# Performance work log

Hardware: AMD Instinct MI355X
Metric: run time of the kernel (lower is better)

The kernel has to match this reference:

```python
import jax, jax.numpy as jnp
import numpy as np

NUM_HEADS = 16


def _rope_tables(seq_len, head_dim, dtype):
    # angles[n, j] = n * 10000^(-2j/head_dim)
    pos = jnp.arange(seq_len, dtype=jnp.float32)
    inv = jnp.power(10000.0, -2.0 * jnp.arange(head_dim // 2, dtype=jnp.float32) / head_dim)
    ang = pos[:, None] * inv[None, :]                     # [N, D/2]
    # repeat_interleave(.., 2): [c0,c0,c1,c1,...]
    cos = jnp.repeat(jnp.cos(ang), 2, axis=-1).astype(dtype)  # [N, D]
    sin = jnp.repeat(jnp.sin(ang), 2, axis=-1).astype(dtype)  # [N, D]
    return cos[None, None], sin[None, None]               # [1,1,N,D]


def _rotate_half_interleaved(x):
    # stack([-x[...,1::2], x[...,::2]], -1).reshape_as(x)
    x2 = jnp.stack([-x[..., 1::2], x[..., ::2]], axis=-1)
    return x2.reshape(x.shape)


def setup_inputs() -> dict:
    key = jax.random.key(0)
    k0, k1, k2, k3 = jax.random.split(key, 4)
    B, N, C = 2, 2048, 1024
    s = 1.0 / np.sqrt(C)
    return {
        "x": jax.random.normal(k0, (B, N, C), dtype=jnp.float32),
        "Wq": jax.random.normal(k1, (C, C), dtype=jnp.float32) * s,
        "Wk": jax.random.normal(k2, (C, C), dtype=jnp.float32) * s,
        "Wv": jax.random.normal(k3, (C, C), dtype=jnp.float32) * s,
    }


def reference(x, Wq, Wk, Wv):
    B, N, C = x.shape
    H = NUM_HEADS
    D = C // H
    scale = D ** -0.5

    def heads(y):  # [B,N,C] -> [B,H,N,D]
        return y.reshape(B, N, H, D).transpose(0, 2, 1, 3)

    # nn.Linear: y = x @ W.T
    q = heads(x @ Wq.T)
    k = heads(x @ Wk.T)
    v = heads(x @ Wv.T)

    cos, sin = _rope_tables(N, D, x.dtype)
    q = q * cos + _rotate_half_interleaved(q) * sin
    k = k * cos + _rotate_half_interleaved(k) * sin

    attn = jnp.einsum("bhnd,bhmd->bhnm", q, k) * scale
    attn = jax.nn.softmax(attn, axis=-1)          # dropout p=0.0 -> identity
    out = jnp.einsum("bhnm,bhmd->bhnd", attn, v)
    return out.transpose(0, 2, 1, 3).reshape(B, N, C)
```

## Files before the change

kernel.cpp:

```cpp
#include <hip/hip_runtime.h>

typedef _Float16 f16;
typedef _Float16 f16x2 __attribute__((ext_vector_type(2)));
typedef _Float16 f16x8 __attribute__((ext_vector_type(8)));
typedef _Float16 f16x4 __attribute__((ext_vector_type(4)));
typedef float f32x4 __attribute__((ext_vector_type(4)));

#define GAS(p) ((const __attribute__((address_space(1))) void*)(p))
#define LAS(p) ((__attribute__((address_space(3))) void*)(p))

__device__ __forceinline__ f32x4 mfma16(f16x8 a, f16x8 b, f32x4 c) {
  return __builtin_amdgcn_mfma_f32_16x16x32_f16(a, b, c, 0, 0, 0);
}

__device__ __forceinline__ f16x2 cvt2(float a, float b) {
  return __builtin_bit_cast(f16x2, __builtin_amdgcn_cvt_pkrtz(a, b));
}

__device__ __forceinline__ void stage_tile(const f16* __restrict__ grow0,
                                           int stride_f16, f16* lds, int t) {
  int r = t >> 3;
  int sw = ((t & 7) ^ (r & 7)) * 8;
  __builtin_amdgcn_global_load_lds(GAS(grow0 + r * stride_f16 + sw),
                                   LAS(lds + t * 8), 16, 0, 0);
}

__global__ void convall(const float* __restrict__ x, const float* __restrict__ wq,
                        const float* __restrict__ wk, const float* __restrict__ wv,
                        f16* __restrict__ xh, f16* __restrict__ wh,
                        float* __restrict__ cosT, float* __restrict__ sinT) {
  int bid = blockIdx.x;
  if (bid >= 3584) {
    int idx = (bid - 3584) * 256 + threadIdx.x;
    int n = idx >> 5, jj = idx & 31;
    float inv = powf(10000.0f, -(float)jj * (1.0f / 32.0f));
    float ang = (float)n * inv;
    cosT[idx] = cosf(ang);
    sinT[idx] = sinf(ang);
    return;
  }
  const float* s;
  f16* d;
  int boff;
  if (bid < 2048)      { s = x;  d = xh;            boff = bid; }
  else if (bid < 2560) { s = wq; d = wh;            boff = bid - 2048; }
  else if (bid < 3072) { s = wk; d = wh + 1048576;  boff = bid - 2560; }
  else                 { s = wv; d = wh + 2097152;  boff = bid - 3072; }
  int i = (boff * 256 + threadIdx.x) * 8;
  float4 a = *(const float4*)(s + i);
  float4 b = *(const float4*)(s + i + 4);
  f16x8 o = {(f16)a.x, (f16)a.y, (f16)a.z, (f16)a.w,
             (f16)b.x, (f16)b.y, (f16)b.z, (f16)b.w};
  *(f16x8*)(d + i) = o;
}

__global__ __launch_bounds__(256, 3) void qkv_gemm(
    const f16* __restrict__ X, const f16* __restrict__ W,
    const float* __restrict__ cosT, const float* __restrict__ sinT,
    f16* __restrict__ Q, f16* __restrict__ K, f16* __restrict__ Vt) {
  __shared__ f16 As[128 * 64];
  __shared__ f16 Bs[128 * 64];
  const int tid = threadIdx.x;
  const int wv = tid >> 6, lane = tid & 63;
  const int m0 = blockIdx.x * 128, n0 = blockIdx.y * 128;
  const int cl = lane & 15, g = lane >> 4;
  const int wr = (wv >> 1) * 64, wc = (wv & 1) * 64;
  const int vx = cl & 7;

  f32x4 acc[4][4] = {};
  const f16* ga = X + (size_t)m0 * 1024;
  const f16* gb = W + (size_t)n0 * 1024;

  for (int kt = 0; kt < 1024; kt += 64) {
    __syncthreads();
#pragma unroll
    for (int rd = 0; rd < 4; ++rd) {
      stage_tile(ga + kt, 1024, As, tid + rd * 256);
      stage_tile(gb + kt, 1024, Bs, tid + rd * 256);
    }
    __syncthreads();
#pragma unroll
    for (int kk = 0; kk < 2; ++kk) {
      f16x8 a[4], bf[4];
#pragma unroll
      for (int mi = 0; mi < 4; ++mi)
        a[mi] = *(const f16x8*)(As + (wr + mi * 16 + cl) * 64 +
                                (((kk * 4 + g) ^ vx) << 3));
#pragma unroll
      for (int ni = 0; ni < 4; ++ni)
        bf[ni] = *(const f16x8*)(Bs + (wc + ni * 16 + cl) * 64 +
                                 (((kk * 4 + g) ^ vx) << 3));
#pragma unroll
      for (int mi = 0; mi < 4; ++mi)
#pragma unroll
        for (int ni = 0; ni < 4; ++ni)
          acc[mi][ni] = mfma16(a[mi], bf[ni], acc[mi][ni]);
    }
  }

  const int p = n0 >> 10;
  for (int mi = 0; mi < 4; ++mi) {
    int rbase = m0 + wr + mi * 16 + g * 4;
    for (int ni = 0; ni < 4; ++ni) {
      int gc = n0 + wc + ni * 16 + cl;
      int f = gc & 1023;
      int h = f >> 6, d = f & 63;
      if (p < 2) {
        int j = d >> 1;
        f16* dst = (p == 0) ? Q : K;
        float sc = (p == 0) ? 0.18033688011f : 1.0f;
        for (int r = 0; r < 4; ++r) {
          int row = rbase + r;
          int bb = row >> 11, n = row & 2047;
          float co = cosT[n * 32 + j], si = sinT[n * 32 + j];
          float v = acc[mi][ni][r];
          float pr = __shfl_xor(v, 1);
          float o = (d & 1) ? (v * co + pr * si) : (v * co - pr * si);
          dst[((bb * 16 + h) * 2048 + n) * 64 + d] = (f16)(o * sc);
        }
      } else {
        int bb = rbase >> 11, n = rbase & 2047;
        int np = (n & ~31) | (((n >> 2) & 3) << 3) | (((n >> 4) & 1) << 2);
        f16x4 pk = {(f16)acc[mi][ni][0], (f16)acc[mi][ni][1],
                    (f16)acc[mi][ni][2], (f16)acc[mi][ni][3]};
        *(f16x4*)(Vt + (size_t)((bb * 16 + h) * 64 + d) * 2048 + np) = pk;
      }
    }
  }
}

__global__ __launch_bounds__(256, 2) void attn(
    const f16* __restrict__ Q, const f16* __restrict__ K,
    const f16* __restrict__ Vt, float* __restrict__ out) {
  __shared__ f16 Ks[2][2][4096];
  __shared__ f16 Vs[2][2][4096];
  const int tid = threadIdx.x;
  const int w = tid >> 6, lane = tid & 63;
  const int cl = lane & 15, g = lane >> 4;
  const int id = blockIdx.x;
  const int xcd = id & 7, j = id >> 3;
  const int bh = xcd * 4 + (j >> 4);
  const int b = bh >> 4, h = bh & 15;
  const int qb = (j & 15) * 128 + w * 32;
  const f16* Qp = Q + (size_t)bh * (2048 * 64);
  const f16* Kp = K + (size_t)bh * (2048 * 64);
  const f16* Vp = Vt + (size_t)bh * (64 * 2048);

  f16x8 bq[2][2];
#pragma unroll
  for (int qh = 0; qh < 2; ++qh) {
    bq[qh][0] = *(const f16x8*)(Qp + (qb + qh * 16 + cl) * 64 + g * 8);
    bq[qh][1] = *(const f16x8*)(Qp + (qb + qh * 16 + cl) * 64 + 32 + g * 8);
  }

  f32x4 acc[2][4] = {};
  float lsp[2] = {0.f, 0.f};
  const int vx = cl & 7;
  const f32x4 z4 = {0.f, 0.f, 0.f, 0.f};
  union PB { f16x8 v; f16x2 hx[4]; };
  struct AS { f32x4 s[2][4]; f16x8 vf[2][4]; };

  auto STAGE = [&](int it, int bf) {
    const f16* kp = Kp + (size_t)it * 8192;
    const f16* vp = Vp + (size_t)it * 128;
#pragma unroll
    for (int hh = 0; hh < 2; ++hh) {
      stage_tile(kp + hh * 4096, 64, Ks[bf][hh], tid);
      stage_tile(kp + hh * 4096, 64, Ks[bf][hh], tid + 256);
      stage_tile(vp + hh * 64, 2048, Vs[bf][hh], tid);
      stage_tile(vp + hh * 64, 2048, Vs[bf][hh], tid + 256);
    }
  };

  auto APH = [&](const f16* kb, const f16* vb, AS& S) {
    f16x8 a0[4], a1[4];
#pragma unroll
    for (int i = 0; i < 4; ++i) {
      const f16* kr = kb + (i * 16 + cl) * 64;
      a0[i] = *(const f16x8*)(kr + ((g ^ vx) << 3));
      a1[i] = *(const f16x8*)(kr + (((4 + g) ^ vx) << 3));
    }
#pragma unroll
    for (int ks = 0; ks < 2; ++ks)
#pragma unroll
      for (int d = 0; d < 4; ++d)
        S.vf[ks][d] = *(const f16x8*)(vb + (d * 16 + cl) * 64 +
                                      (((ks * 4 + g) ^ vx) << 3));
    __builtin_amdgcn_s_setprio(1);
#pragma unroll
    for (int qh = 0; qh < 2; ++qh)
#pragma unroll
      for (int i = 0; i < 4; ++i)
        S.s[qh][i] = mfma16(a1[i], bq[qh][1], mfma16(a0[i], bq[qh][0], z4));
    __builtin_amdgcn_s_setprio(0);
  };

  auto BPH = [&](AS& S) {
    PB pb[2][2];
#pragma unroll
    for (int qh = 0; qh < 2; ++qh) {
      float p0 = exp2f(S.s[qh][0][0]), p1 = exp2f(S.s[qh][0][1]);
      float p2 = exp2f(S.s[qh][0][2]), p3 = exp2f(S.s[qh][0][3]);
      float p4 = exp2f(S.s[qh][1][0]), p5 = exp2f(S.s[qh][1][1]);
      float p6 = exp2f(S.s[qh][1][2]), p7 = exp2f(S.s[qh][1][3]);
      float p8 = exp2f(S.s[qh][2][0]), p9 = exp2f(S.s[qh][2][1]);
      float pa = exp2f(S.s[qh][2][2]), pc = exp2f(S.s[qh][2][3]);
      float pd = exp2f(S.s[qh][3][0]), pe = exp2f(S.s[qh][3][1]);
      float pf = exp2f(S.s[qh][3][2]), pg = exp2f(S.s[qh][3][3]);
      lsp[qh] += (((p0 + p1) + (p2 + p3)) + ((p4 + p5) + (p6 + p7))) +
                 (((p8 + p9) + (pa + pc)) + ((pd + pe) + (pf + pg)));
      pb[qh][0].hx[0] = cvt2(p0, p1); pb[qh][0].hx[1] = cvt2(p2, p3);
      pb[qh][0].hx[2] = cvt2(p4, p5); pb[qh][0].hx[3] = cvt2(p6, p7);
      pb[qh][1].hx[0] = cvt2(p8, p9); pb[qh][1].hx[1] = cvt2(pa, pc);
      pb[qh][1].hx[2] = cvt2(pd, pe); pb[qh][1].hx[3] = cvt2(pf, pg);
    }
    __builtin_amdgcn_s_setprio(1);
#pragma unroll
    for (int ks = 0; ks < 2; ++ks)
#pragma unroll
      for (int d = 0; d < 4; ++d) {
        acc[0][d] = mfma16(S.vf[ks][d], pb[0][ks].v, acc[0][d]);
        acc[1][d] = mfma16(S.vf[ks][d], pb[1][ks].v, acc[1][d]);
      }
    __builtin_amdgcn_s_setprio(0);
  };

  STAGE(0, 0);
  asm volatile("s_waitcnt vmcnt(0)" ::: "memory");
  __builtin_amdgcn_s_barrier();
  STAGE(1, 1);
  AS P, Qs;
  APH(Ks[0][0], Vs[0][0], P);

  for (int it = 0; it < 16; ++it) {
    const int c = it & 1;
    APH(Ks[c][1], Vs[c][1], Qs);
    BPH(P);
    if (it < 15) {
      asm volatile("s_waitcnt vmcnt(0)" ::: "memory");
      __builtin_amdgcn_s_barrier();
      if (it + 2 < 16) STAGE(it + 2, c);
      APH(Ks[c ^ 1][0], Vs[c ^ 1][0], P);
      BPH(Qs);
    } else {
      BPH(Qs);
    }
  }

#pragma unroll
  for (int qh = 0; qh < 2; ++qh) {
    float ls = lsp[qh];
    ls += __shfl_xor(ls, 16);
    ls += __shfl_xor(ls, 32);
    float inv = 1.0f / ls;
    float* ob = out + (size_t)(b * 2048 + qb + qh * 16 + cl) * 1024 +
                h * 64 + g * 4;
#pragma unroll
    for (int d = 0; d < 4; ++d) {
      float4 o = {acc[qh][d][0] * inv, acc[qh][d][1] * inv,
                  acc[qh][d][2] * inv, acc[qh][d][3] * inv};
      *(float4*)(ob + (size_t)d * 16) = o;
    }
  }
}

extern "C" void kernel_launch(void* const* d_in, const int* in_sizes, int n_in,
                              void* d_out, int out_size, void* d_ws, size_t ws_size,
                              hipStream_t stream) {
  const float* x  = (const float*)d_in[0];
  const float* Wq = (const float*)d_in[1];
  const float* Wk = (const float*)d_in[2];
  const float* Wv = (const float*)d_in[3];
  float* out = (float*)d_out;
  char* ws = (char*)d_ws;

  f16* xh   = (f16*)(ws);
  f16* wh   = (f16*)(ws + 8388608);
  f16* Qr   = (f16*)(ws + 14680064);
  f16* Kr   = (f16*)(ws + 23068672);
  f16* Vt   = (f16*)(ws + 31457280);
  float* cosT = (float*)(ws + 39845888);
  float* sinT = (float*)(ws + 40108032);

  convall<<<3840, 256, 0, stream>>>(x, Wq, Wk, Wv, xh, wh, cosT, sinT);

  dim3 g1(32, 24);
  qkv_gemm<<<g1, 256, 0, stream>>>(xh, wh, cosT, sinT, Qr, Kr, Vt);

  attn<<<512, 256, 0, stream>>>(Qr, Kr, Vt, out);
}
```

Baseline: 97.23 us.

## Load V fragments directly from global memory and enlarge K LDS tiles

V-transposed fragments are now read straight from global memory into registers inside the score phase, so V no longer goes through LDS. The freed LDS holds K tiles of 256 keys, which halves the number of barrier-synchronized stages to 8 iterations of four 64-key sub-tiles. The intent is to cut LDS traffic and barrier count. The cost is that the global V loads are strided by 2048 per row with no swizzle, and their latency is exposed unless the K pipelining hides it.

```diff
diff --git a/kernel.cpp b/kernel.cpp
--- a/kernel.cpp
+++ b/kernel.cpp
@@ -132,8 +132,7 @@
 __global__ __launch_bounds__(256, 2) void attn(
     const f16* __restrict__ Q, const f16* __restrict__ K,
     const f16* __restrict__ Vt, float* __restrict__ out) {
-  __shared__ f16 Ks[2][2][4096];
-  __shared__ f16 Vs[2][2][4096];
+  __shared__ f16 Ks[2][4][4096];
   const int tid = threadIdx.x;
   const int w = tid >> 6, lane = tid & 63;
   const int cl = lane & 15, g = lane >> 4;
@@ -159,20 +158,24 @@
   const f32x4 z4 = {0.f, 0.f, 0.f, 0.f};
   union PB { f16x8 v; f16x2 hx[4]; };
   struct AS { f32x4 s[2][4]; f16x8 vf[2][4]; };
+  const f16* vbase = Vp + (size_t)cl * 2048 + g * 8;
 
   auto STAGE = [&](int it, int bf) {
-    const f16* kp = Kp + (size_t)it * 8192;
-    const f16* vp = Vp + (size_t)it * 128;
-#pragma unroll
-    for (int hh = 0; hh < 2; ++hh) {
-      stage_tile(kp + hh * 4096, 64, Ks[bf][hh], tid);
-      stage_tile(kp + hh * 4096, 64, Ks[bf][hh], tid + 256);
-      stage_tile(vp + hh * 64, 2048, Vs[bf][hh], tid);
-      stage_tile(vp + hh * 64, 2048, Vs[bf][hh], tid + 256);
+    const f16* kp = Kp + (size_t)it * 16384;
+#pragma unroll
+    for (int sub = 0; sub < 4; ++sub) {
+      stage_tile(kp + sub * 4096, 64, Ks[bf][sub], tid);
+      stage_tile(kp + sub * 4096, 64, Ks[bf][sub], tid + 256);
     }
   };
 
-  auto APH = [&](const f16* kb, const f16* vb, AS& S) {
+  auto APH = [&](const f16* kb, int kt2, AS& S) {
+    const f16* vp = vbase + kt2;
+#pragma unroll
+    for (int ks = 0; ks < 2; ++ks)
+#pragma unroll
+      for (int d = 0; d < 4; ++d)
+        S.vf[ks][d] = *(const f16x8*)(vp + (size_t)d * 32768 + ks * 32);
     f16x8 a0[4], a1[4];
 #pragma unroll
     for (int i = 0; i < 4; ++i) {
@@ -180,12 +183,6 @@
       a0[i] = *(const f16x8*)(kr + ((g ^ vx) << 3));
       a1[i] = *(const f16x8*)(kr + (((4 + g) ^ vx) << 3));
     }
-#pragma unroll
-    for (int ks = 0; ks < 2; ++ks)
-#pragma unroll
-      for (int d = 0; d < 4; ++d)
-        S.vf[ks][d] = *(const f16x8*)(vb + (d * 16 + cl) * 64 +
-                                      (((ks * 4 + g) ^ vx) << 3));
     __builtin_amdgcn_s_setprio(1);
 #pragma unroll
     for (int qh = 0; qh < 2; ++qh)
@@ -226,25 +223,22 @@
   };
 
   STAGE(0, 0);
-  asm volatile("s_waitcnt vmcnt(0)" ::: "memory");
-  __builtin_amdgcn_s_barrier();
-  STAGE(1, 1);
-  AS P, Qs;
-  APH(Ks[0][0], Vs[0][0], P);
-
-  for (int it = 0; it < 16; ++it) {
-    const int c = it & 1;
-    APH(Ks[c][1], Vs[c][1], Qs);
+  AS P, Q2;
+  int cur = 0;
+  for (int it = 0; it < 8; ++it) {
+    const int kt = it * 256;
+    asm volatile("s_waitcnt vmcnt(0)" ::: "memory");
+    __builtin_amdgcn_s_barrier();
+    if (it + 1 < 8) STAGE(it + 1, cur ^ 1);
+    APH(Ks[cur][0], kt, P);
+    APH(Ks[cur][1], kt + 64, Q2);
     BPH(P);
-    if (it < 15) {
-      asm volatile("s_waitcnt vmcnt(0)" ::: "memory");
-      __builtin_amdgcn_s_barrier();
-      if (it + 2 < 16) STAGE(it + 2, c);
-      APH(Ks[c ^ 1][0], Vs[c ^ 1][0], P);
-      BPH(Qs);
-    } else {
-      BPH(Qs);
-    }
+    APH(Ks[cur][2], kt + 128, P);
+    BPH(Q2);
+    APH(Ks[cur][3], kt + 192, Q2);
+    BPH(P);
+    BPH(Q2);
+    cur ^= 1;
   }
 
 #pragma unroll
```

New measurement: 124.4 us. 27.9% more time.
